# Kernel optimization log

Measured on AMD Instinct MI355X. Metric: run time of the kernel, lower is better.

## Reference

```python
import jax, jax.numpy as jnp
import numpy as np
import math

B, L, H, E = 4, 2048, 16, 64

def setup_inputs() -> dict:
    key = jax.random.key(0)
    kq, kk, kv = jax.random.split(key, 3)
    queries = jax.random.normal(kq, (B, L, H, E), dtype=jnp.float32)
    keys = jax.random.normal(kk, (B, L, H, E), dtype=jnp.float32)
    values = jax.random.normal(kv, (B, L, H, E), dtype=jnp.float32)
    return {"queries": queries, "keys": keys, "values": values}

def reference(queries, keys, values):
    # queries: [B,L,H,E], keys: [B,S,H,E], values: [B,S,H,D]
    Bq, Lq, Hq, Eq = queries.shape
    scale = 1.0 / math.sqrt(Eq)
    scores = jnp.einsum('blhe,bshe->bhls', queries, keys)  # [B,H,L,S]
    Sq = keys.shape[1]
    causal = jnp.triu(jnp.ones((Lq, Sq), dtype=bool), k=1)  # True above diagonal
    scores = jnp.where(causal[None, None], -jnp.inf, scores)
    A = jax.nn.softmax(scale * scores, axis=-1)  # dropout is identity in eval
    V = jnp.einsum('bhls,bshd->blhd', A, values)
    return V
```

## Files before the change

kernel.cpp:

```cpp
#include <hip/hip_runtime.h>
#include <hip/hip_bf16.h>

typedef __attribute__((ext_vector_type(8))) short bf16x8;
typedef __attribute__((ext_vector_type(4))) short bf16x4;
typedef __attribute__((ext_vector_type(4))) float f32x4;
typedef __attribute__((ext_vector_type(16))) float f32x16;

#define NB 4
#define NL 2048
#define NH 16
#define NE 64
#define HE (NH*NE)
#define QW 32
#define QBLK 128
#define NQT (NL/QBLK)
#define NPAIR (NQT/2)
#define NBH 64
#define NKT 32
#define TILE_IMG 16384
#define WS_NEED ((size_t)NBH * NKT * TILE_IMG)
#define QSCALE (0.125f * 1.44269504088896340736f)

union Pfrag { unsigned u[4]; bf16x8 v; };

__device__ __forceinline__ unsigned pk2(float a, float b) {
  float2 t; t.x = a; t.y = b;
  __hip_bfloat162 hh = __float22bfloat162_rn(t);
  union { __hip_bfloat162 h; unsigned u; } v; v.h = hh;
  return v.u;
}
#if defined(__has_builtin) && __has_builtin(__builtin_amdgcn_exp2f)
__device__ __forceinline__ float fast_exp2(float x) {
  return __builtin_amdgcn_exp2f(x);
}
#else
__device__ __forceinline__ float fast_exp2(float x) { return exp2f(x); }
#endif
__device__ __forceinline__ void pswap(unsigned &a, unsigned &b) {
  auto r = __builtin_amdgcn_permlane32_swap(a, b, false, false);
  a = r[0]; b = r[1];
}
#define SWZ(row,col) ((row)*128 + ((col) ^ ((((row) ^ ((row)>>2)) & 7) << 4)))

__device__ __forceinline__ void cp16(unsigned char* lds, const unsigned char* g) {
  __builtin_amdgcn_global_load_lds(
      (const __attribute__((address_space(1))) unsigned int*)g,
      (__attribute__((address_space(3))) unsigned int*)lds, 16, 0, 0);
}

__global__ __launch_bounds__(256) void fa_stage(
    const float* __restrict__ K, const float* __restrict__ V,
    unsigned char* __restrict__ img)
{
  const int tid = threadIdx.x;
  const int bid = blockIdx.x;
  const int bh  = bid >> 5;
  const int t0  = bid & 31;
  const int h = bh & (NH-1), b = bh >> 4;
  const size_t base = ((size_t)b * NL * NH + h) * NE + (size_t)(t0 * 64) * HE;
  unsigned char* kimg = img + (size_t)(bh * NKT + t0) * TILE_IMG;
  unsigned char* vimg = kimg + 8192;
  #pragma unroll
  for (int rep = 0; rep < 2; ++rep) {
    const int idx = rep * 256 + tid;
    const int row = idx >> 3, gr = idx & 7;
    const float* kp = K + base + (size_t)row * HE + gr * 8;
    f32x4 a0 = *(const f32x4*)kp;
    f32x4 a1 = *(const f32x4*)(kp + 4);
    Pfrag w;
    w.u[0] = pk2(a0[0], a0[1]); w.u[1] = pk2(a0[2], a0[3]);
    w.u[2] = pk2(a1[0], a1[1]); w.u[3] = pk2(a1[2], a1[3]);
    *(bf16x8*)(kimg + SWZ(row, gr * 16)) = w.v;
  }
  const int trow = tid >> 4, tcol = (tid & 15) * 4, sq = trow * 4;
  f32x4 vr[4];
  #pragma unroll
  for (int i = 0; i < 4; ++i)
    vr[i] = *(const f32x4*)(V + base + (size_t)(sq + i) * HE + tcol);
  #pragma unroll
  for (int j = 0; j < 4; ++j) {
    const int er = tcol + j;
    union { unsigned u[2]; bf16x4 v; } w;
    w.u[0] = pk2(vr[0][j], vr[1][j]);
    w.u[1] = pk2(vr[2][j], vr[3][j]);
    *(bf16x4*)(vimg + SWZ(er, sq * 2)) = w.v;
  }
}

#define PACK(SC, PA0, PA1)                                                     \
      {                                                                        \
        unsigned c0 = pk2(SC[0],SC[1]),   c1 = pk2(SC[2],SC[3]);               \
        unsigned c2 = pk2(SC[4],SC[5]),   c3 = pk2(SC[6],SC[7]);               \
        unsigned c4 = pk2(SC[8],SC[9]),   c5 = pk2(SC[10],SC[11]);             \
        unsigned c6 = pk2(SC[12],SC[13]), c7 = pk2(SC[14],SC[15]);             \
        pswap(c0, c2);  pswap(c1, c3);                                         \
        pswap(c4, c6);  pswap(c5, c7);                                         \
        PA0.u[0]=c0; PA0.u[1]=c1; PA0.u[2]=c2; PA0.u[3]=c3;                    \
        PA1.u[0]=c4; PA1.u[1]=c5; PA1.u[2]=c6; PA1.u[3]=c7;                    \
      }                                                                        \
      l_acc = __builtin_amdgcn_mfma_f32_32x32x16_bf16(ones.v, PA0.v, l_acc,0,0,0);\
      l_acc = __builtin_amdgcn_mfma_f32_32x32x16_bf16(ones.v, PA1.v, l_acc,0,0,0);

#define SMPACK(SC, PA0, PA1)                                                   \
      _Pragma("unroll")                                                        \
      for (int r = 0; r < 16; ++r) SC[r] = fast_exp2(SC[r]);                   \
      PACK(SC, PA0, PA1)

#define PVSTEP(VBUF)                                                           \
    {                                                                          \
      _Pragma("unroll")                                                        \
      for (int dt = 0; dt < 2; ++dt) {                                         \
        bf16x8 v00 = *(const bf16x8*)(&v_lds[VBUF][0] + addr4[0] + dt*4096);   \
        bf16x8 v01 = *(const bf16x8*)(&v_lds[VBUF][0] + addr4[1] + dt*4096);   \
        bf16x8 v10 = *(const bf16x8*)(&v_lds[VBUF][0] + addr4[2] + dt*4096);   \
        bf16x8 v11 = *(const bf16x8*)(&v_lds[VBUF][0] + addr4[3] + dt*4096);   \
        oacc2[0][dt] = __builtin_amdgcn_mfma_f32_32x32x16_bf16(                \
            v00, p00.v, oacc2[0][dt], 0, 0, 0);                                \
        oacc2[1][dt] = __builtin_amdgcn_mfma_f32_32x32x16_bf16(                \
            v10, p10.v, oacc2[1][dt], 0, 0, 0);                                \
        oacc2[0][dt] = __builtin_amdgcn_mfma_f32_32x32x16_bf16(                \
            v01, p01.v, oacc2[0][dt], 0, 0, 0);                                \
        oacc2[1][dt] = __builtin_amdgcn_mfma_f32_32x32x16_bf16(                \
            v11, p11.v, oacc2[1][dt], 0, 0, 0);                                \
      }                                                                        \
    }

#define STEP(IT, BUF)                                                          \
    {                                                                          \
      if ((IT) + 1 < nt) { asm volatile("s_waitcnt vmcnt(4)" ::: "memory"); }  \
      else               { asm volatile("s_waitcnt vmcnt(0)" ::: "memory"); }  \
      __builtin_amdgcn_sched_barrier(0);                                       \
      __builtin_amdgcn_s_barrier();                                            \
      __builtin_amdgcn_sched_barrier(0);                                       \
      if ((IT) + 2 < nt) {                                                     \
        unsigned char* kd = &k_lds[((BUF)+2)&3][0];                            \
        unsigned char* vd = &v_lds[((BUF)+2)&3][0];                            \
        cp16(kd + wb,        src_pf);                                          \
        cp16(kd + 4096 + wb, src_pf + 4096);                                   \
        cp16(vd + wb,        src_pf + 8192);                                   \
        cp16(vd + 4096 + wb, src_pf + 12288);                                  \
        src_pf += TILE_IMG;                                                    \
      }                                                                        \
      Pfrag n00, n01, n10, n11;                                                \
      const int kv0 = (IT)*64;                                                 \
      if (kv0 + 63 <= qb) {                                                    \
        f32x16 sc0 = (f32x16)0.0f, sc1 = (f32x16)0.0f;                         \
        _Pragma("unroll")                                                      \
        for (int ks = 0; ks < 4; ++ks) {                                       \
          bf16x8 af0 = *(const bf16x8*)(&k_lds[BUF][0] + addr4[ks]);           \
          bf16x8 af1 = *(const bf16x8*)(&k_lds[BUF][0] + addr4[ks] + 4096);    \
          sc0 = __builtin_amdgcn_mfma_f32_32x32x16_bf16(af0, qf[ks], sc0,0,0,0);\
          sc1 = __builtin_amdgcn_mfma_f32_32x32x16_bf16(af1, qf[ks], sc1,0,0,0);\
        }                                                                      \
        SMPACK(sc0, n00, n01)                                                  \
        SMPACK(sc1, n10, n11)                                                  \
      } else {                                                                 \
        if (kv0 <= qb + 31) {                                                  \
          f32x16 sc = (f32x16)0.0f;                                            \
          _Pragma("unroll")                                                    \
          for (int ks = 0; ks < 4; ++ks) {                                     \
            bf16x8 af = *(const bf16x8*)(&k_lds[BUF][0] + addr4[ks]);          \
            sc = __builtin_amdgcn_mfma_f32_32x32x16_bf16(af, qf[ks], sc,0,0,0);\
          }                                                                    \
          _Pragma("unroll")                                                    \
          for (int r = 0; r < 16; ++r) {                                       \
            const int kvg = kv0 + (r&3) + 8*(r>>2) + 4*hi;                     \
            sc[r] = (kvg > qg) ? 0.0f : fast_exp2(sc[r]);                      \
          }                                                                    \
          PACK(sc, n00, n01)                                                   \
        } else {                                                               \
          n00.u[0]=0; n00.u[1]=0; n00.u[2]=0; n00.u[3]=0;                      \
          n01.u[0]=0; n01.u[1]=0; n01.u[2]=0; n01.u[3]=0;                      \
        }                                                                      \
        if (kv0 + 32 <= qb + 31) {                                             \
          f32x16 sc = (f32x16)0.0f;                                            \
          _Pragma("unroll")                                                    \
          for (int ks = 0; ks < 4; ++ks) {                                     \
            bf16x8 af = *(const bf16x8*)(&k_lds[BUF][0] + addr4[ks] + 4096);   \
            sc = __builtin_amdgcn_mfma_f32_32x32x16_bf16(af, qf[ks], sc,0,0,0);\
          }                                                                    \
          _Pragma("unroll")                                                    \
          for (int r = 0; r < 16; ++r) {                                       \
            const int kvg = kv0 + 32 + (r&3) + 8*(r>>2) + 4*hi;                \
            sc[r] = (kvg > qg) ? 0.0f : fast_exp2(sc[r]);                      \
          }                                                                    \
          PACK(sc, n10, n11)                                                   \
        } else {                                                               \
          n10.u[0]=0; n10.u[1]=0; n10.u[2]=0; n10.u[3]=0;                      \
          n11.u[0]=0; n11.u[1]=0; n11.u[2]=0; n11.u[3]=0;                      \
        }                                                                      \
      }                                                                        \
      if ((IT) > 0) PVSTEP(((BUF)+3)&3)                                        \
      p00 = n00; p01 = n01; p10 = n10; p11 = n11;                              \
    }

#define QTILE_SETUP()                                                          \
    bf16x8 qf[4];                                                              \
    {                                                                          \
      const float* qp = Qb + (size_t)(qb + ln) * HE + hi * 8;                  \
      _Pragma("unroll")                                                        \
      for (int ks = 0; ks < 4; ++ks) {                                         \
        f32x4 a0 = *(const f32x4*)(qp + ks*16);                                \
        f32x4 a1 = *(const f32x4*)(qp + ks*16 + 4);                            \
        Pfrag f;                                                               \
        f.u[0] = pk2(a0[0]*QSCALE, a0[1]*QSCALE);                              \
        f.u[1] = pk2(a0[2]*QSCALE, a0[3]*QSCALE);                              \
        f.u[2] = pk2(a1[0]*QSCALE, a1[1]*QSCALE);                              \
        f.u[3] = pk2(a1[2]*QSCALE, a1[3]*QSCALE);                              \
        qf[ks] = f.v;                                                          \
      }                                                                        \
    }                                                                          \
    f32x16 oacc2[2][2];                                                        \
    oacc2[0][0] = (f32x16)0.0f; oacc2[0][1] = (f32x16)0.0f;                    \
    oacc2[1][0] = (f32x16)0.0f; oacc2[1][1] = (f32x16)0.0f;                    \
    f32x16 l_acc = (f32x16)0.0f;                                               \
    Pfrag p00, p01, p10, p11;                                                  \
    p00.u[0]=0;p00.u[1]=0;p00.u[2]=0;p00.u[3]=0;                               \
    p01=p00; p10=p00; p11=p00;

__global__ __launch_bounds__(256, 2) void fa_fwd(
    const float* __restrict__ Q, const unsigned char* __restrict__ img,
    float* __restrict__ O)
{
  __shared__ unsigned char k_lds[4][8192];
  __shared__ unsigned char v_lds[4][8192];

  const int tid  = threadIdx.x;
  const int lane = tid & 63;
  const int wid  = tid >> 6;
  const int hi   = lane >> 5;
  const int ln   = lane & 31;

  const int bidp = blockIdx.x;
  const int lb   = (bidp & 7) * 64 + (bidp >> 3);
  const int pair = lb & 7;
  const int bh   = lb >> 3;
  const int h    = bh & (NH-1);
  const int b    = bh >> 4;

  const size_t base = ((size_t)b * NL * NH + h) * NE;
  const float* Qb = Q + base;
  float*       Ob = O + base;
  const unsigned char* bimg = img + (size_t)bh * NKT * TILE_IMG;

  int addr4[4];
  {
    const int F = ((ln ^ (ln >> 2)) & 7) << 4;
    #pragma unroll
    for (int j = 0; j < 4; ++j) addr4[j] = ln*128 + ((j*32 + hi*16) ^ F);
  }
  const int wb = wid << 10;

  Pfrag ones;
  ones.u[0] = 0x3F803F80u; ones.u[1] = 0x3F803F80u;
  ones.u[2] = 0x3F803F80u; ones.u[3] = 0x3F803F80u;

  #pragma unroll 1
  for (int hf = 0; hf < 2; ++hf) {
    const int qt = hf ? (NQT - 1 - pair) : pair;
    const int q0 = qt * QBLK;
    const int qb = q0 + wid * QW;
    const int nt = qt * 2 + 2;
    const int qg = qb + ln;

    QTILE_SETUP()

    asm volatile("s_waitcnt vmcnt(0)" ::: "memory");
    __builtin_amdgcn_sched_barrier(0);
    __builtin_amdgcn_s_barrier();
    const unsigned char* src_pf = bimg + (size_t)tid * 16;
    cp16(&k_lds[0][0] + wb,        src_pf);
    cp16(&k_lds[0][0] + 4096 + wb, src_pf + 4096);
    cp16(&v_lds[0][0] + wb,        src_pf + 8192);
    cp16(&v_lds[0][0] + 4096 + wb, src_pf + 12288);
    src_pf += TILE_IMG;
    cp16(&k_lds[1][0] + wb,        src_pf);
    cp16(&k_lds[1][0] + 4096 + wb, src_pf + 4096);
    cp16(&v_lds[1][0] + wb,        src_pf + 8192);
    cp16(&v_lds[1][0] + 4096 + wb, src_pf + 12288);
    src_pf += TILE_IMG;

    int bs = 0;
    #pragma unroll 1
    for (; bs + 4 <= nt; bs += 4) {
      STEP(bs + 0, 0)
      STEP(bs + 1, 1)
      STEP(bs + 2, 2)
      STEP(bs + 3, 3)
    }
    if (bs < nt) {
      STEP(bs + 0, 0)
      STEP(bs + 1, 1)
    }
    PVSTEP((nt + 3) & 3)

    const float inv = 1.0f / l_acc[0];
    float* op = Ob + (size_t)(qb + ln) * HE;
    #pragma unroll
    for (int dt = 0; dt < 2; ++dt)
      #pragma unroll
      for (int rq = 0; rq < 4; ++rq) {
        f32x4 w;
        w[0]=(oacc2[0][dt][rq*4+0]+oacc2[1][dt][rq*4+0])*inv;
        w[1]=(oacc2[0][dt][rq*4+1]+oacc2[1][dt][rq*4+1])*inv;
        w[2]=(oacc2[0][dt][rq*4+2]+oacc2[1][dt][rq*4+2])*inv;
        w[3]=(oacc2[0][dt][rq*4+3]+oacc2[1][dt][rq*4+3])*inv;
        *(f32x4*)(op + dt*32 + 8*rq + 4*hi) = w;
      }
  }
}

__global__ __launch_bounds__(256, 3) void fa_fwd_fused(
    const float* __restrict__ Q, const float* __restrict__ K,
    const float* __restrict__ V, float* __restrict__ O)
{
  __shared__ unsigned char kf_lds[2][64*128];
  __shared__ unsigned char vf_lds[2][64*128];
  const int tid  = threadIdx.x;
  const int lane = tid & 63;
  const int wid  = tid >> 6;
  const int hi   = lane >> 5;
  const int ln   = lane & 31;
  const int trow = tid >> 4;
  const int tcol = (tid & 15) * 4;
  const int sq   = trow * 4;
  const int bidp = blockIdx.x;
  const int lb   = (bidp & 7) * 64 + (bidp >> 3);
  const int pair = lb & 7;
  const int bh   = lb >> 3;
  const int h    = bh & (NH-1);
  const int b    = bh >> 4;
  const size_t base = ((size_t)b * NL * NH + h) * NE;
  const float* Qb = Q + base;
  const float* Kb = K + base;
  const float* Vb = V + base;
  float*       Ob = O + base;
  int cur = 0;
  #pragma unroll 1
  for (int hf = 0; hf < 2; ++hf) {
    const int qt = hf ? (NQT - 1 - pair) : pair;
    const int q0 = qt * QBLK;
    const int qb = q0 + wid * QW;
    const int nt = qt * 2 + 2;
    const int qg = qb + ln;
    bf16x8 qf[4];
    {
      const float* qp = Qb + (size_t)(qb + ln) * HE + hi * 8;
      #pragma unroll
      for (int ks = 0; ks < 4; ++ks) {
        f32x4 a0 = *(const f32x4*)(qp + ks*16);
        f32x4 a1 = *(const f32x4*)(qp + ks*16 + 4);
        Pfrag f;
        f.u[0] = pk2(a0[0]*QSCALE, a0[1]*QSCALE);
        f.u[1] = pk2(a0[2]*QSCALE, a0[3]*QSCALE);
        f.u[2] = pk2(a1[0]*QSCALE, a1[1]*QSCALE);
        f.u[3] = pk2(a1[2]*QSCALE, a1[3]*QSCALE);
        qf[ks] = f.v;
      }
    }
    f32x16 oacc[2];
    oacc[0] = (f32x16)0.0f; oacc[1] = (f32x16)0.0f;
    float l_run = 0.0f;
    f32x4 kreg[4], vreg[4];
    #pragma unroll
    for (int p = 0; p < 4; ++p)
      kreg[p] = *(const f32x4*)(Kb + (size_t)(trow + p*16) * HE + tcol);
    #pragma unroll
    for (int i = 0; i < 4; ++i)
      vreg[i] = *(const f32x4*)(Vb + (size_t)(sq + i) * HE + tcol);
    #pragma unroll 1
    for (int it = 0; it < nt; ++it) {
      unsigned char* kb = kf_lds[cur];
      unsigned char* vb = vf_lds[cur];
      #pragma unroll
      for (int p = 0; p < 4; ++p) {
        const int row = trow + p*16;
        union { unsigned u[2]; bf16x4 v; } w;
        w.u[0] = pk2(kreg[p][0], kreg[p][1]);
        w.u[1] = pk2(kreg[p][2], kreg[p][3]);
        *(bf16x4*)(kb + SWZ(row, tcol*2)) = w.v;
      }
      #pragma unroll
      for (int j = 0; j < 4; ++j) {
        const int er = tcol + j;
        union { unsigned u[2]; bf16x4 v; } w;
        w.u[0] = pk2(vreg[0][j], vreg[1][j]);
        w.u[1] = pk2(vreg[2][j], vreg[3][j]);
        *(bf16x4*)(vb + SWZ(er, sq*2)) = w.v;
      }
      if (it + 1 < nt) {
        const int s0 = (it + 1) * 64;
        #pragma unroll
        for (int p = 0; p < 4; ++p)
          kreg[p] = *(const f32x4*)(Kb + (size_t)(s0 + trow + p*16) * HE + tcol);
        #pragma unroll
        for (int i = 0; i < 4; ++i)
          vreg[i] = *(const f32x4*)(Vb + (size_t)(s0 + sq + i) * HE + tcol);
      }
      asm volatile("s_waitcnt lgkmcnt(0)" ::: "memory");
      __builtin_amdgcn_sched_barrier(0);
      __builtin_amdgcn_s_barrier();
      __builtin_amdgcn_sched_barrier(0);
      #pragma unroll
      for (int sub = 0; sub < 2; ++sub) {
        const int kv0s = it*64 + sub*32;
        if (kv0s <= qb + QW - 1) {
          f32x16 sc = (f32x16)0.0f;
          #pragma unroll
          for (int ks = 0; ks < 4; ++ks) {
            const int kvr = sub*32 + ln;
            bf16x8 af = *(const bf16x8*)(kb + SWZ(kvr, ks*32 + hi*16));
            sc = __builtin_amdgcn_mfma_f32_32x32x16_bf16(af, qf[ks], sc, 0, 0, 0);
          }
          if (kv0s + 31 > qb) {
            #pragma unroll
            for (int r = 0; r < 16; ++r) {
              const int kvg = kv0s + (r&3) + 8*(r>>2) + 4*hi;
              sc[r] = (kvg > qg) ? 0.0f : fast_exp2(sc[r]);
            }
          } else {
            #pragma unroll
            for (int r = 0; r < 16; ++r) sc[r] = fast_exp2(sc[r]);
          }
          float s0_ = (sc[0]+sc[1])+(sc[2]+sc[3]);
          float s1_ = (sc[4]+sc[5])+(sc[6]+sc[7]);
          float s2_ = (sc[8]+sc[9])+(sc[10]+sc[11]);
          float s3_ = (sc[12]+sc[13])+(sc[14]+sc[15]);
          float ls = (s0_+s1_)+(s2_+s3_);
          ls += __shfl_xor(ls, 32);
          l_run += ls;
          unsigned c0 = pk2(sc[0],sc[1]),   c1 = pk2(sc[2],sc[3]);
          unsigned c2 = pk2(sc[4],sc[5]),   c3 = pk2(sc[6],sc[7]);
          unsigned c4 = pk2(sc[8],sc[9]),   c5 = pk2(sc[10],sc[11]);
          unsigned c6 = pk2(sc[12],sc[13]), c7 = pk2(sc[14],sc[15]);
          pswap(c0, c2);  pswap(c1, c3);
          pswap(c4, c6);  pswap(c5, c7);
          Pfrag pa0, pa1;
          pa0.u[0]=c0; pa0.u[1]=c1; pa0.u[2]=c2; pa0.u[3]=c3;
          pa1.u[0]=c4; pa1.u[1]=c5; pa1.u[2]=c6; pa1.u[3]=c7;
          #pragma unroll
          for (int dt = 0; dt < 2; ++dt) {
            const int dr = dt*32 + ln;
            #pragma unroll
            for (int ks2 = 0; ks2 < 2; ++ks2) {
              bf16x8 av = *(const bf16x8*)(vb + SWZ(dr, sub*64 + ks2*32 + hi*16));
              oacc[dt] = __builtin_amdgcn_mfma_f32_32x32x16_bf16(
                  av, ks2 ? pa1.v : pa0.v, oacc[dt], 0, 0, 0);
            }
          }
        }
      }
      cur ^= 1;
    }
    const float inv = 1.0f / l_run;
    float* op = Ob + (size_t)(qb + ln) * HE;
    #pragma unroll
    for (int dt = 0; dt < 2; ++dt)
      #pragma unroll
      for (int rq = 0; rq < 4; ++rq) {
        f32x4 w;
        w[0]=oacc[dt][rq*4+0]*inv; w[1]=oacc[dt][rq*4+1]*inv;
        w[2]=oacc[dt][rq*4+2]*inv; w[3]=oacc[dt][rq*4+3]*inv;
        *(f32x4*)(op + dt*32 + 8*rq + 4*hi) = w;
      }
  }
}

extern "C" void kernel_launch(void* const* d_in, const int* in_sizes, int n_in,
                              void* d_out, int out_size, void* d_ws, size_t ws_size,
                              hipStream_t stream) {
  const float* Q = (const float*)d_in[0];
  const float* K = (const float*)d_in[1];
  const float* V = (const float*)d_in[2];
  float* O = (float*)d_out;
  if (ws_size >= WS_NEED) {
    fa_stage<<<dim3(NBH * NKT), dim3(256), 0, stream>>>(K, V, (unsigned char*)d_ws);
    fa_fwd<<<dim3(NB * NH * NPAIR), dim3(256), 0, stream>>>(
        Q, (const unsigned char*)d_ws, O);
  } else {
    fa_fwd_fused<<<dim3(NB * NH * NPAIR), dim3(256), 0, stream>>>(Q, K, V, O);
  }
}
```

Baseline: 72.31 us.

## Launch one block per query tile, triple-buffer KV, compute row sums with VALU

The paired-tile persistent loop is replaced by one block per (batch-head, query tile), launched heaviest tile first, and occupancy is raised to 3 blocks per CU. The K/V LDS ring shrinks from four to three stages. V fragments are now loaded into registers during the current step and consumed by the PV MFMAs of the next step. The ones-matrix MFMA for the softmax denominator is replaced by scalar adds plus a cross-half shuffle, and one output accumulator pair is dropped to cut register use. The costs are more blocks to schedule, a shallower prefetch ring, and extra lgkmcnt waits.

```diff
diff --git a/kernel.cpp b/kernel.cpp
--- a/kernel.cpp
+++ b/kernel.cpp
@@ -14,7 +14,6 @@
 #define QW 32
 #define QBLK 128
 #define NQT (NL/QBLK)
-#define NPAIR (NQT/2)
 #define NBH 64
 #define NKT 32
 #define TILE_IMG 16384
@@ -97,69 +96,73 @@
         pswap(c4, c6);  pswap(c5, c7);                                         \
         PA0.u[0]=c0; PA0.u[1]=c1; PA0.u[2]=c2; PA0.u[3]=c3;                    \
         PA1.u[0]=c4; PA1.u[1]=c5; PA1.u[2]=c6; PA1.u[3]=c7;                    \
-      }                                                                        \
-      l_acc = __builtin_amdgcn_mfma_f32_32x32x16_bf16(ones.v, PA0.v, l_acc,0,0,0);\
-      l_acc = __builtin_amdgcn_mfma_f32_32x32x16_bf16(ones.v, PA1.v, l_acc,0,0,0);
+      }
+
+#define LSUM(SC)                                                               \
+      l_run += ((((SC[0]+SC[1])+(SC[2]+SC[3]))+((SC[4]+SC[5])+(SC[6]+SC[7])))  \
+             + (((SC[8]+SC[9])+(SC[10]+SC[11]))+((SC[12]+SC[13])+(SC[14]+SC[15]))));
 
 #define SMPACK(SC, PA0, PA1)                                                   \
       _Pragma("unroll")                                                        \
       for (int r = 0; r < 16; ++r) SC[r] = fast_exp2(SC[r]);                   \
+      LSUM(SC)                                                                 \
       PACK(SC, PA0, PA1)
 
-#define PVSTEP(VBUF)                                                           \
+#define PVPREV()                                                               \
     {                                                                          \
       _Pragma("unroll")                                                        \
       for (int dt = 0; dt < 2; ++dt) {                                         \
-        bf16x8 v00 = *(const bf16x8*)(&v_lds[VBUF][0] + addr4[0] + dt*4096);   \
-        bf16x8 v01 = *(const bf16x8*)(&v_lds[VBUF][0] + addr4[1] + dt*4096);   \
-        bf16x8 v10 = *(const bf16x8*)(&v_lds[VBUF][0] + addr4[2] + dt*4096);   \
-        bf16x8 v11 = *(const bf16x8*)(&v_lds[VBUF][0] + addr4[3] + dt*4096);   \
-        oacc2[0][dt] = __builtin_amdgcn_mfma_f32_32x32x16_bf16(                \
-            v00, p00.v, oacc2[0][dt], 0, 0, 0);                                \
-        oacc2[1][dt] = __builtin_amdgcn_mfma_f32_32x32x16_bf16(                \
-            v10, p10.v, oacc2[1][dt], 0, 0, 0);                                \
-        oacc2[0][dt] = __builtin_amdgcn_mfma_f32_32x32x16_bf16(                \
-            v01, p01.v, oacc2[0][dt], 0, 0, 0);                                \
-        oacc2[1][dt] = __builtin_amdgcn_mfma_f32_32x32x16_bf16(                \
-            v11, p11.v, oacc2[1][dt], 0, 0, 0);                                \
+        oacc[dt] = __builtin_amdgcn_mfma_f32_32x32x16_bf16(                    \
+            vv[0][dt], p00.v, oacc[dt], 0, 0, 0);                              \
+        oacc[dt] = __builtin_amdgcn_mfma_f32_32x32x16_bf16(                    \
+            vv[2][dt], p10.v, oacc[dt], 0, 0, 0);                              \
+        oacc[dt] = __builtin_amdgcn_mfma_f32_32x32x16_bf16(                    \
+            vv[1][dt], p01.v, oacc[dt], 0, 0, 0);                              \
+        oacc[dt] = __builtin_amdgcn_mfma_f32_32x32x16_bf16(                    \
+            vv[3][dt], p11.v, oacc[dt], 0, 0, 0);                              \
       }                                                                        \
     }
 
 #define STEP(IT, BUF)                                                          \
     {                                                                          \
-      if ((IT) + 1 < nt) { asm volatile("s_waitcnt vmcnt(4)" ::: "memory"); }  \
-      else               { asm volatile("s_waitcnt vmcnt(0)" ::: "memory"); }  \
+      if ((IT) + 1 < nt) {                                                     \
+        asm volatile("s_waitcnt vmcnt(4) lgkmcnt(0)" ::: "memory");            \
+      } else {                                                                 \
+        asm volatile("s_waitcnt vmcnt(0) lgkmcnt(0)" ::: "memory");            \
+      }                                                                        \
       __builtin_amdgcn_sched_barrier(0);                                       \
       __builtin_amdgcn_s_barrier();                                            \
       __builtin_amdgcn_sched_barrier(0);                                       \
       if ((IT) + 2 < nt) {                                                     \
-        unsigned char* kd = &k_lds[((BUF)+2)&3][0];                            \
-        unsigned char* vd = &v_lds[((BUF)+2)&3][0];                            \
+        unsigned char* kd = &k_lds[((BUF)+2)%3][0];                            \
+        unsigned char* vd = &v_lds[((BUF)+2)%3][0];                            \
         cp16(kd + wb,        src_pf);                                          \
         cp16(kd + 4096 + wb, src_pf + 4096);                                   \
         cp16(vd + wb,        src_pf + 8192);                                   \
         cp16(vd + 4096 + wb, src_pf + 12288);                                  \
         src_pf += TILE_IMG;                                                    \
       }                                                                        \
-      Pfrag n00, n01, n10, n11;                                                \
+      if ((IT) > 0) PVPREV()                                                   \
+      const unsigned char* kb = &k_lds[BUF][0];                                \
+      const unsigned char* vbp = &v_lds[BUF][0];                               \
       const int kv0 = (IT)*64;                                                 \
       if (kv0 + 63 <= qb) {                                                    \
         f32x16 sc0 = (f32x16)0.0f, sc1 = (f32x16)0.0f;                         \
         _Pragma("unroll")                                                      \
         for (int ks = 0; ks < 4; ++ks) {                                       \
-          bf16x8 af0 = *(const bf16x8*)(&k_lds[BUF][0] + addr4[ks]);           \
-          bf16x8 af1 = *(const bf16x8*)(&k_lds[BUF][0] + addr4[ks] + 4096);    \
+          bf16x8 af0 = *(const bf16x8*)(kb + addr4[ks]);                       \
+          bf16x8 af1 = *(const bf16x8*)(kb + addr4[ks] + 4096);                \
           sc0 = __builtin_amdgcn_mfma_f32_32x32x16_bf16(af0, qf[ks], sc0,0,0,0);\
           sc1 = __builtin_amdgcn_mfma_f32_32x32x16_bf16(af1, qf[ks], sc1,0,0,0);\
         }                                                                      \
-        SMPACK(sc0, n00, n01)                                                  \
-        SMPACK(sc1, n10, n11)                                                  \
+        SMPACK(sc0, p00, p01)                                                  \
+        SMPACK(sc1, p10, p11)                                                  \
       } else {                                                                 \
         if (kv0 <= qb + 31) {                                                  \
           f32x16 sc = (f32x16)0.0f;                                            \
           _Pragma("unroll")                                                    \
           for (int ks = 0; ks < 4; ++ks) {                                     \
-            bf16x8 af = *(const bf16x8*)(&k_lds[BUF][0] + addr4[ks]);          \
+            bf16x8 af = *(const bf16x8*)(kb + addr4[ks]);                      \
             sc = __builtin_amdgcn_mfma_f32_32x32x16_bf16(af, qf[ks], sc,0,0,0);\
           }                                                                    \
           _Pragma("unroll")                                                    \
@@ -167,16 +170,16 @@
             const int kvg = kv0 + (r&3) + 8*(r>>2) + 4*hi;                     \
             sc[r] = (kvg > qg) ? 0.0f : fast_exp2(sc[r]);                      \
           }                                                                    \
-          PACK(sc, n00, n01)                                                   \
+          LSUM(sc)                                                             \
+          PACK(sc, p00, p01)                                                   \
         } else {                                                               \
-          n00.u[0]=0; n00.u[1]=0; n00.u[2]=0; n00.u[3]=0;                      \
-          n01.u[0]=0; n01.u[1]=0; n01.u[2]=0; n01.u[3]=0;                      \
+          p00.u[0]=0; p00.u[1]=0; p00.u[2]=0; p00.u[3]=0; p01 = p00;           \
         }                                                                      \
         if (kv0 + 32 <= qb + 31) {                                             \
           f32x16 sc = (f32x16)0.0f;                                            \
           _Pragma("unroll")                                                    \
           for (int ks = 0; ks < 4; ++ks) {                                     \
-            bf16x8 af = *(const bf16x8*)(&k_lds[BUF][0] + addr4[ks] + 4096);   \
+            bf16x8 af = *(const bf16x8*)(kb + addr4[ks] + 4096);               \
             sc = __builtin_amdgcn_mfma_f32_32x32x16_bf16(af, qf[ks], sc,0,0,0);\
           }                                                                    \
           _Pragma("unroll")                                                    \
@@ -184,46 +187,25 @@
             const int kvg = kv0 + 32 + (r&3) + 8*(r>>2) + 4*hi;                \
             sc[r] = (kvg > qg) ? 0.0f : fast_exp2(sc[r]);                      \
           }                                                                    \
-          PACK(sc, n10, n11)                                                   \
+          LSUM(sc)                                                             \
+          PACK(sc, p10, p11)                                                   \
         } else {                                                               \
-          n10.u[0]=0; n10.u[1]=0; n10.u[2]=0; n10.u[3]=0;                      \
-          n11.u[0]=0; n11.u[1]=0; n11.u[2]=0; n11.u[3]=0;                      \
+          p10.u[0]=0; p10.u[1]=0; p10.u[2]=0; p10.u[3]=0; p11 = p10;           \
         }                                                                      \
       }                                                                        \
-      if ((IT) > 0) PVSTEP(((BUF)+3)&3)                                        \
-      p00 = n00; p01 = n01; p10 = n10; p11 = n11;                              \
-    }
-
-#define QTILE_SETUP()                                                          \
-    bf16x8 qf[4];                                                              \
-    {                                                                          \
-      const float* qp = Qb + (size_t)(qb + ln) * HE + hi * 8;                  \
       _Pragma("unroll")                                                        \
-      for (int ks = 0; ks < 4; ++ks) {                                         \
-        f32x4 a0 = *(const f32x4*)(qp + ks*16);                                \
-        f32x4 a1 = *(const f32x4*)(qp + ks*16 + 4);                            \
-        Pfrag f;                                                               \
-        f.u[0] = pk2(a0[0]*QSCALE, a0[1]*QSCALE);                              \
-        f.u[1] = pk2(a0[2]*QSCALE, a0[3]*QSCALE);                              \
-        f.u[2] = pk2(a1[0]*QSCALE, a1[1]*QSCALE);                              \
-        f.u[3] = pk2(a1[2]*QSCALE, a1[3]*QSCALE);                              \
-        qf[ks] = f.v;                                                          \
+      for (int j = 0; j < 4; ++j) {                                            \
+        vv[j][0] = *(const bf16x8*)(vbp + addr4[j]);                           \
+        vv[j][1] = *(const bf16x8*)(vbp + addr4[j] + 4096);                    \
       }                                                                        \
-    }                                                                          \
-    f32x16 oacc2[2][2];                                                        \
-    oacc2[0][0] = (f32x16)0.0f; oacc2[0][1] = (f32x16)0.0f;                    \
-    oacc2[1][0] = (f32x16)0.0f; oacc2[1][1] = (f32x16)0.0f;                    \
-    f32x16 l_acc = (f32x16)0.0f;                                               \
-    Pfrag p00, p01, p10, p11;                                                  \
-    p00.u[0]=0;p00.u[1]=0;p00.u[2]=0;p00.u[3]=0;                               \
-    p01=p00; p10=p00; p11=p00;
-
-__global__ __launch_bounds__(256, 2) void fa_fwd(
+    }
+
+__global__ __launch_bounds__(256, 3) void fa_fwd(
     const float* __restrict__ Q, const unsigned char* __restrict__ img,
     float* __restrict__ O)
 {
-  __shared__ unsigned char k_lds[4][8192];
-  __shared__ unsigned char v_lds[4][8192];
+  __shared__ unsigned char k_lds[3][8192];
+  __shared__ unsigned char v_lds[3][8192];
 
   const int tid  = threadIdx.x;
   const int lane = tid & 63;
@@ -231,12 +213,11 @@
   const int hi   = lane >> 5;
   const int ln   = lane & 31;
 
-  const int bidp = blockIdx.x;
-  const int lb   = (bidp & 7) * 64 + (bidp >> 3);
-  const int pair = lb & 7;
-  const int bh   = lb >> 3;
-  const int h    = bh & (NH-1);
-  const int b    = bh >> 4;
+  const int bid = blockIdx.x;
+  const int bh  = bid & 63;
+  const int qt  = (NQT - 1) - (bid >> 6);
+  const int h   = bh & (NH-1);
+  const int b   = bh >> 4;
 
   const size_t base = ((size_t)b * NL * NH + h) * NE;
   const float* Qb = Q + base;
@@ -251,63 +232,73 @@
   }
   const int wb = wid << 10;
 
-  Pfrag ones;
-  ones.u[0] = 0x3F803F80u; ones.u[1] = 0x3F803F80u;
-  ones.u[2] = 0x3F803F80u; ones.u[3] = 0x3F803F80u;
-
+  const int q0 = qt * QBLK;
+  const int qb = q0 + wid * QW;
+  const int nt = qt * 2 + 2;
+  const int qg = qb + ln;
+
+  bf16x8 qf[4];
+  {
+    const float* qp = Qb + (size_t)(qb + ln) * HE + hi * 8;
+    #pragma unroll
+    for (int ks = 0; ks < 4; ++ks) {
+      f32x4 a0 = *(const f32x4*)(qp + ks*16);
+      f32x4 a1 = *(const f32x4*)(qp + ks*16 + 4);
+      Pfrag f;
+      f.u[0] = pk2(a0[0]*QSCALE, a0[1]*QSCALE);
+      f.u[1] = pk2(a0[2]*QSCALE, a0[3]*QSCALE);
+      f.u[2] = pk2(a1[0]*QSCALE, a1[1]*QSCALE);
+      f.u[3] = pk2(a1[2]*QSCALE, a1[3]*QSCALE);
+      qf[ks] = f.v;
+    }
+  }
+  f32x16 oacc[2];
+  oacc[0] = (f32x16)0.0f; oacc[1] = (f32x16)0.0f;
+  float l_run = 0.0f;
+  Pfrag p00, p01, p10, p11;
+  p00.u[0]=0;p00.u[1]=0;p00.u[2]=0;p00.u[3]=0; p01=p00; p10=p00; p11=p00;
+  bf16x8 vv[4][2];
+
+  asm volatile("s_waitcnt vmcnt(0)" ::: "memory");
+  __builtin_amdgcn_sched_barrier(0);
+  const unsigned char* src_pf = bimg + (size_t)tid * 16;
+  cp16(&k_lds[0][0] + wb,        src_pf);
+  cp16(&k_lds[0][0] + 4096 + wb, src_pf + 4096);
+  cp16(&v_lds[0][0] + wb,        src_pf + 8192);
+  cp16(&v_lds[0][0] + 4096 + wb, src_pf + 12288);
+  src_pf += TILE_IMG;
+  cp16(&k_lds[1][0] + wb,        src_pf);
+  cp16(&k_lds[1][0] + 4096 + wb, src_pf + 4096);
+  cp16(&v_lds[1][0] + wb,        src_pf + 8192);
+  cp16(&v_lds[1][0] + 4096 + wb, src_pf + 12288);
+  src_pf += TILE_IMG;
+
+  int it0 = 0;
   #pragma unroll 1
-  for (int hf = 0; hf < 2; ++hf) {
-    const int qt = hf ? (NQT - 1 - pair) : pair;
-    const int q0 = qt * QBLK;
-    const int qb = q0 + wid * QW;
-    const int nt = qt * 2 + 2;
-    const int qg = qb + ln;
-
-    QTILE_SETUP()
-
-    asm volatile("s_waitcnt vmcnt(0)" ::: "memory");
-    __builtin_amdgcn_sched_barrier(0);
-    __builtin_amdgcn_s_barrier();
-    const unsigned char* src_pf = bimg + (size_t)tid * 16;
-    cp16(&k_lds[0][0] + wb,        src_pf);
-    cp16(&k_lds[0][0] + 4096 + wb, src_pf + 4096);
-    cp16(&v_lds[0][0] + wb,        src_pf + 8192);
-    cp16(&v_lds[0][0] + 4096 + wb, src_pf + 12288);
-    src_pf += TILE_IMG;
-    cp16(&k_lds[1][0] + wb,        src_pf);
-    cp16(&k_lds[1][0] + 4096 + wb, src_pf + 4096);
-    cp16(&v_lds[1][0] + wb,        src_pf + 8192);
-    cp16(&v_lds[1][0] + 4096 + wb, src_pf + 12288);
-    src_pf += TILE_IMG;
-
-    int bs = 0;
-    #pragma unroll 1
-    for (; bs + 4 <= nt; bs += 4) {
-      STEP(bs + 0, 0)
-      STEP(bs + 1, 1)
-      STEP(bs + 2, 2)
-      STEP(bs + 3, 3)
-    }
-    if (bs < nt) {
-      STEP(bs + 0, 0)
-      STEP(bs + 1, 1)
-    }
-    PVSTEP((nt + 3) & 3)
-
-    const float inv = 1.0f / l_acc[0];
-    float* op = Ob + (size_t)(qb + ln) * HE;
-    #pragma unroll
-    for (int dt = 0; dt < 2; ++dt)
-      #pragma unroll
-      for (int rq = 0; rq < 4; ++rq) {
-        f32x4 w;
-        w[0]=(oacc2[0][dt][rq*4+0]+oacc2[1][dt][rq*4+0])*inv;
-        w[1]=(oacc2[0][dt][rq*4+1]+oacc2[1][dt][rq*4+1])*inv;
-        w[2]=(oacc2[0][dt][rq*4+2]+oacc2[1][dt][rq*4+2])*inv;
-        w[3]=(oacc2[0][dt][rq*4+3]+oacc2[1][dt][rq*4+3])*inv;
-        *(f32x4*)(op + dt*32 + 8*rq + 4*hi) = w;
-      }
-  }
+  for (; it0 + 3 <= nt; it0 += 3) {
+    STEP(it0 + 0, 0)
+    STEP(it0 + 1, 1)
+    STEP(it0 + 2, 2)
+  }
+  {
+    const int rem = nt - it0;
+    if (rem >= 1) STEP(it0, 0)
+    if (rem == 2) STEP(it0 + 1, 1)
+  }
+  PVPREV()
+
+  const float l_tot = l_run + __shfl_xor(l_run, 32);
+  const float inv = 1.0f / l_tot;
+  float* op = Ob + (size_t)(qb + ln) * HE;
+  #pragma unroll
+  for (int dt = 0; dt < 2; ++dt)
+    #pragma unroll
+    for (int rq = 0; rq < 4; ++rq) {
+      f32x4 w;
+      w[0]=oacc[dt][rq*4+0]*inv; w[1]=oacc[dt][rq*4+1]*inv;
+      w[2]=oacc[dt][rq*4+2]*inv; w[3]=oacc[dt][rq*4+3]*inv;
+      *(f32x4*)(op + dt*32 + 8*rq + 4*hi) = w;
+    }
 }
 
 __global__ __launch_bounds__(256, 3) void fa_fwd_fused(
@@ -475,9 +466,9 @@
   float* O = (float*)d_out;
   if (ws_size >= WS_NEED) {
     fa_stage<<<dim3(NBH * NKT), dim3(256), 0, stream>>>(K, V, (unsigned char*)d_ws);
-    fa_fwd<<<dim3(NB * NH * NPAIR), dim3(256), 0, stream>>>(
+    fa_fwd<<<dim3(NBH * NQT), dim3(256), 0, stream>>>(
         Q, (const unsigned char*)d_ws, O);
   } else {
-    fa_fwd_fused<<<dim3(NB * NH * NPAIR), dim3(256), 0, stream>>>(Q, K, V, O);
-  }
-}
+    fa_fwd_fused<<<dim3(NB * NH * 8), dim3(256), 0, stream>>>(Q, K, V, O);
+  }
+}
```

Result: no change. 71.75 us (-0.8%).
